# Kernel optimization log

Hardware: AMD Instinct MI355X
Metric: run time of the kernel (lower is better)

The kernel has to match this reference:

```python
import jax, jax.numpy as jnp
import numpy as np

N_SRC1, N_TGT1, N_TGT2 = 200000, 50000, 10000
E1, E2 = 1000000, 300000
F_IN, F_HID, F_OUT = 256, 192, 128


def setup_inputs() -> dict:
    key = jax.random.key(0)
    ks = jax.random.split(key, 16)
    x = jax.random.normal(ks[0], (N_SRC1, F_IN), dtype=jnp.float32)
    ei1 = jnp.stack([
        jax.random.randint(ks[1], (E1,), 0, N_SRC1, dtype=jnp.int32),
        jax.random.randint(ks[2], (E1,), 0, N_TGT1, dtype=jnp.int32),
    ])
    ei2 = jnp.stack([
        jax.random.randint(ks[3], (E2,), 0, N_TGT1, dtype=jnp.int32),
        jax.random.randint(ks[4], (E2,), 0, N_TGT2, dtype=jnp.int32),
    ])
    def w(k, o, i):
        return jax.random.normal(k, (o, i), dtype=jnp.float32) * (1.0 / np.sqrt(i))
    return {
        "x": x, "ei1": ei1, "ei2": ei2,
        "Wl1": w(ks[5], F_HID, F_IN), "bl1": jnp.zeros((F_HID,), jnp.float32), "Wr1": w(ks[6], F_HID, F_IN),
        "Wl2": w(ks[7], F_HID, F_HID), "bl2": jnp.zeros((F_HID,), jnp.float32), "Wr2": w(ks[8], F_HID, F_HID),
        "W1": w(ks[9], F_HID, F_HID), "b1": jnp.zeros((F_HID,), jnp.float32),
        "W2": w(ks[10], F_OUT, F_HID), "b2": jnp.zeros((F_OUT,), jnp.float32),
    }


def _segment_mean(feat, tgt, n):
    s = jax.ops.segment_sum(feat, tgt, num_segments=n)  # [n, d]
    c = jax.ops.segment_sum(jnp.ones((tgt.shape[0], 1), feat.dtype), tgt, num_segments=n)
    return s / jnp.maximum(c, 1.0)


def _sage_conv(x, ei, n_tgt, Wl, bl, Wr):
    # PyG SAGEConv (mean aggr): lin_l(mean of src feats per tgt) + lin_r(x_target)
    agg = _segment_mean(x[ei[0]], ei[1], n_tgt)
    return agg @ Wl.T + bl + x[:n_tgt] @ Wr.T


def reference(x, ei1, ei2, Wl1, bl1, Wr1, Wl2, bl2, Wr2, W1, b1, W2, b2):
    h = jax.nn.relu(_sage_conv(x, ei1, N_TGT1, Wl1, bl1, Wr1))   # dropout is identity in eval
    h = jax.nn.relu(_sage_conv(h, ei2, N_TGT2, Wl2, bl2, Wr2))
    embedding = h @ W1.T + b1
    h = jax.nn.relu(embedding)
    logits = h @ W2.T + b2
    return jax.nn.log_softmax(logits, axis=-1), embedding
```

## Files before the change

### kernel.cpp

```cpp
#include <hip/hip_runtime.h>
#include <hip/hip_bf16.h>

#define N_SRC1 200000
#define N_TGT1 50000
#define N_TGT2 10000
#define E1_N   1000000
#define E2_N   300000
#define F_IN   256
#define F_HID  192
#define F_OUT  128

typedef __attribute__((ext_vector_type(4))) float f32x4;
typedef __attribute__((ext_vector_type(8))) short short8;

__device__ inline float bf2f(ushort u) {
    union { uint i; float f; } c; c.i = ((uint)u) << 16; return c.f;
}
__device__ inline ushort f2bf(float f) {
    union { float f; uint i; } c; c.f = f;
    uint u = c.i;
    return (ushort)((u + 0x7FFFu + ((u >> 16) & 1u)) >> 16);
}
__device__ inline uint pack2(float a, float b) {
    return (uint)f2bf(a) | ((uint)f2bf(b) << 16);
}

#define HB1 3907
#define HB2 1172

__global__ __launch_bounds__(256) void prep(
    const float4* __restrict__ x4, uint2* __restrict__ xb,
    const float* __restrict__ Wl1, const float* __restrict__ Wr1,
    const float* __restrict__ Wl2, const float* __restrict__ Wr2,
    const float* __restrict__ W1, const float* __restrict__ W2,
    ushort* __restrict__ wc1, ushort* __restrict__ wc2,
    ushort* __restrict__ w1b, ushort* __restrict__ w2b)
{
    const int b = blockIdx.x, tid = threadIdx.x;
    if (b < 2048) {
        const int n4 = N_SRC1 * F_IN / 4;
        for (int i = b * 256 + tid; i < n4; i += 2048 * 256) {
            float4 v = x4[i];
            uint2 o;
            o.x = pack2(v.x, v.y);
            o.y = pack2(v.z, v.w);
            xb[i] = o;
        }
        return;
    }
    const int wt = (b - 2048) * 256 + tid;
    for (int idx = wt; idx < 233472; idx += 128 * 256) {
        if (idx < 98304) {
            int n = idx >> 9, k = idx & 511;
            float v = (k < 256) ? Wl1[n * 256 + k] : Wr1[n * 256 + (k - 256)];
            wc1[idx] = f2bf(v);
        } else if (idx < 98304 + 73728) {
            int i2 = idx - 98304;
            int n = i2 / 384, k = i2 - n * 384;
            float v = (k < 192) ? Wl2[n * 192 + k] : Wr2[n * 192 + (k - 192)];
            wc2[i2] = f2bf(v);
        } else if (idx < 98304 + 73728 + 36864) {
            int i3 = idx - (98304 + 73728);
            w1b[i3] = f2bf(W1[i3]);
        } else {
            int i4 = idx - (98304 + 73728 + 36864);
            w2b[i4] = f2bf(W2[i4]);
        }
    }
}

__global__ __launch_bounds__(256) void hist_kernel(
    const int* __restrict__ tgt, int* __restrict__ cnt, int E)
{
    int i = blockIdx.x * blockDim.x + threadIdx.x;
    if (i < E) atomicAdd(cnt + tgt[i], 1);
}

__global__ __launch_bounds__(256) void scan_blocks(
    const int* __restrict__ cnt, int n, int* __restrict__ off,
    int* __restrict__ partials)
{
    __shared__ int s[256];
    int tid = threadIdx.x;
    int i = blockIdx.x * 256 + tid;
    int v = (i < n) ? cnt[i] : 0;
    s[tid] = v;
    __syncthreads();
#pragma unroll
    for (int o = 1; o < 256; o <<= 1) {
        int t = (tid >= o) ? s[tid - o] : 0;
        __syncthreads();
        s[tid] += t;
        __syncthreads();
    }
    if (i < n) off[i] = s[tid] - v;
    if (tid == 255) partials[blockIdx.x] = s[255];
}

__global__ __launch_bounds__(256) void scan_partials_block(
    int* __restrict__ partials, int np, int* __restrict__ total_out)
{
    __shared__ int s[256];
    int tid = threadIdx.x;
    int v = (tid < np) ? partials[tid] : 0;
    s[tid] = v;
    __syncthreads();
#pragma unroll
    for (int o = 1; o < 256; o <<= 1) {
        int t = (tid >= o) ? s[tid - o] : 0;
        __syncthreads();
        s[tid] += t;
        __syncthreads();
    }
    if (tid < np) partials[tid] = s[tid] - v;
    if (tid == 255) *total_out = s[255];
}

__global__ __launch_bounds__(256) void add_off(
    int* __restrict__ off, const int* __restrict__ partials,
    int* __restrict__ cur, int n)
{
    int i = blockIdx.x * blockDim.x + threadIdx.x;
    if (i < n) {
        int v = off[i] + partials[i >> 8];
        off[i] = v;
        cur[i] = v;
    }
}

__global__ __launch_bounds__(256) void fill_edges(
    const int* __restrict__ src, const int* __restrict__ tgt,
    int* __restrict__ cur, int* __restrict__ esrc, int E)
{
    int i = blockIdx.x * blockDim.x + threadIdx.x;
    if (i < E) {
        int pos = atomicAdd(cur + tgt[i], 1);
        esrc[pos] = src[i];
    }
}

__global__ __launch_bounds__(256) void aggregate_bf16_256(
    const int* __restrict__ esrc, const int* __restrict__ off,
    const ushort* __restrict__ X, ushort* __restrict__ seg, int n)
{
    int wid  = blockIdx.x * 4 + (threadIdx.x >> 6);
    int lane = threadIdx.x & 63;
    if (wid >= n) return;
    int s0 = off[wid], s1 = off[wid + 1];
    float a0 = 0, a1 = 0, a2 = 0, a3 = 0;
    const uint2* base = (const uint2*)X;
    int e = s0;
    for (; e + 4 <= s1; e += 4) {
        int i0 = esrc[e], i1 = esrc[e + 1], i2 = esrc[e + 2], i3 = esrc[e + 3];
        uint2 v0 = base[(size_t)i0 * 64 + lane];
        uint2 v1 = base[(size_t)i1 * 64 + lane];
        uint2 v2 = base[(size_t)i2 * 64 + lane];
        uint2 v3 = base[(size_t)i3 * 64 + lane];
        a0 += bf2f((ushort)(v0.x & 0xffff)) + bf2f((ushort)(v1.x & 0xffff))
            + bf2f((ushort)(v2.x & 0xffff)) + bf2f((ushort)(v3.x & 0xffff));
        a1 += bf2f((ushort)(v0.x >> 16)) + bf2f((ushort)(v1.x >> 16))
            + bf2f((ushort)(v2.x >> 16)) + bf2f((ushort)(v3.x >> 16));
        a2 += bf2f((ushort)(v0.y & 0xffff)) + bf2f((ushort)(v1.y & 0xffff))
            + bf2f((ushort)(v2.y & 0xffff)) + bf2f((ushort)(v3.y & 0xffff));
        a3 += bf2f((ushort)(v0.y >> 16)) + bf2f((ushort)(v1.y >> 16))
            + bf2f((ushort)(v2.y >> 16)) + bf2f((ushort)(v3.y >> 16));
    }
    for (; e < s1; ++e) {
        uint2 v = base[(size_t)esrc[e] * 64 + lane];
        a0 += bf2f((ushort)(v.x & 0xffff)); a1 += bf2f((ushort)(v.x >> 16));
        a2 += bf2f((ushort)(v.y & 0xffff)); a3 += bf2f((ushort)(v.y >> 16));
    }
    float inv = (s1 > s0) ? 1.0f / (float)(s1 - s0) : 0.0f;
    uint2 o;
    o.x = pack2(a0 * inv, a1 * inv);
    o.y = pack2(a2 * inv, a3 * inv);
    ((uint2*)seg)[(size_t)wid * 64 + lane] = o;
}

__global__ __launch_bounds__(256) void aggregate_bf16_192(
    const int* __restrict__ esrc, const int* __restrict__ off,
    const ushort* __restrict__ X, ushort* __restrict__ seg, int n)
{
    int wid  = blockIdx.x * 4 + (threadIdx.x >> 6);
    int lane = threadIdx.x & 63;
    if (wid >= n) return;
    int s0 = off[wid], s1 = off[wid + 1];
    float a0 = 0, a1 = 0, a2 = 0, a3 = 0;
    const uint* base = (const uint*)X;
    int e = s0;
    for (; e + 4 <= s1; e += 4) {
        const uint* r0 = base + (size_t)esrc[e] * 96;
        const uint* r1 = base + (size_t)esrc[e + 1] * 96;
        const uint* r2 = base + (size_t)esrc[e + 2] * 96;
        const uint* r3 = base + (size_t)esrc[e + 3] * 96;
        uint w0 = r0[lane], w1 = r1[lane], w2 = r2[lane], w3 = r3[lane];
        a0 += bf2f((ushort)(w0 & 0xffff)) + bf2f((ushort)(w1 & 0xffff))
            + bf2f((ushort)(w2 & 0xffff)) + bf2f((ushort)(w3 & 0xffff));
        a1 += bf2f((ushort)(w0 >> 16)) + bf2f((ushort)(w1 >> 16))
            + bf2f((ushort)(w2 >> 16)) + bf2f((ushort)(w3 >> 16));
        if (lane < 32) {
            uint u0 = r0[64 + lane], u1 = r1[64 + lane],
                 u2 = r2[64 + lane], u3 = r3[64 + lane];
            a2 += bf2f((ushort)(u0 & 0xffff)) + bf2f((ushort)(u1 & 0xffff))
                + bf2f((ushort)(u2 & 0xffff)) + bf2f((ushort)(u3 & 0xffff));
            a3 += bf2f((ushort)(u0 >> 16)) + bf2f((ushort)(u1 >> 16))
                + bf2f((ushort)(u2 >> 16)) + bf2f((ushort)(u3 >> 16));
        }
    }
    for (; e < s1; ++e) {
        const uint* r = base + (size_t)esrc[e] * 96;
        uint v0 = r[lane];
        a0 += bf2f((ushort)(v0 & 0xffff)); a1 += bf2f((ushort)(v0 >> 16));
        if (lane < 32) {
            uint v1 = r[64 + lane];
            a2 += bf2f((ushort)(v1 & 0xffff)); a3 += bf2f((ushort)(v1 >> 16));
        }
    }
    float inv = (s1 > s0) ? 1.0f / (float)(s1 - s0) : 0.0f;
    uint* o = (uint*)seg + (size_t)wid * 96;
    o[lane] = pack2(a0 * inv, a1 * inv);
    if (lane < 32) o[64 + lane] = pack2(a2 * inv, a3 * inv);
}

template <int BM, int BN, int WM, int WN>
__global__ __launch_bounds__(WM * WN * 64) void gemm_mfma(
    const ushort* __restrict__ A1, int K1,
    const ushort* __restrict__ A2, int K2,
    const ushort* __restrict__ W, const float* __restrict__ bias,
    ushort* __restrict__ Cb, float* __restrict__ Cf,
    int M, int relu)
{
    constexpr int TPB = WM * WN * 64;
    constexpr int WTM = BM / WM, WTN = BN / WN;
    constexpr int MF = WTM / 16, NF = WTN / 16;
    constexpr int ROW = 40;
    __shared__ __attribute__((aligned(16))) ushort As[BM * ROW];
    __shared__ __attribute__((aligned(16))) ushort Ws[BN * ROW];
    const int tid  = threadIdx.x;
    const int lane = tid & 63;
    const int wid  = tid >> 6;
    const int wm = wid / WN, wn = wid % WN;
    const int bm = blockIdx.x * BM;
    const int K = K1 + K2;

    f32x4 acc[MF][NF];
#pragma unroll
    for (int i = 0; i < MF; ++i)
#pragma unroll
        for (int j = 0; j < NF; ++j) acc[i][j] = {0.f, 0.f, 0.f, 0.f};

    for (int k0 = 0; k0 < K; k0 += 32) {
#pragma unroll
        for (int c = tid; c < BM * 4; c += TPB) {
            int row = c >> 2, k8 = (c & 3) * 8;
            int m = bm + row, k = k0 + k8;
            uint4 v = make_uint4(0, 0, 0, 0);
            if (m < M) {
                const ushort* s = (k < K1) ? (A1 + (size_t)m * K1 + k)
                                           : (A2 + (size_t)m * K2 + (k - K1));
                v = *(const uint4*)s;
            }
            *(uint4*)&As[row * ROW + k8] = v;
        }
#pragma unroll
        for (int c = tid; c < BN * 4; c += TPB) {
            int row = c >> 2, k8 = (c & 3) * 8;
            uint4 v = *(const uint4*)(W + (size_t)row * K + k0 + k8);
            *(uint4*)&Ws[row * ROW + k8] = v;
        }
        __syncthreads();
        short8 a[MF], b[NF];
#pragma unroll
        for (int mf = 0; mf < MF; ++mf)
            a[mf] = *(const short8*)&As[(wm * WTM + mf * 16 + (lane & 15)) * ROW + (lane >> 4) * 8];
#pragma unroll
        for (int nf = 0; nf < NF; ++nf)
            b[nf] = *(const short8*)&Ws[(wn * WTN + nf * 16 + (lane & 15)) * ROW + (lane >> 4) * 8];
#pragma unroll
        for (int mf = 0; mf < MF; ++mf)
#pragma unroll
            for (int nf = 0; nf < NF; ++nf)
                acc[mf][nf] = __builtin_amdgcn_mfma_f32_16x16x32_bf16(
                    a[mf], b[nf], acc[mf][nf], 0, 0, 0);
        __syncthreads();
    }

#pragma unroll
    for (int mf = 0; mf < MF; ++mf) {
        int r0 = bm + wm * WTM + mf * 16 + (lane >> 4) * 4;
#pragma unroll
        for (int nf = 0; nf < NF; ++nf) {
            int cc = wn * WTN + nf * 16 + (lane & 15);
            float bi = bias[cc];
#pragma unroll
            for (int r = 0; r < 4; ++r) {
                int m = r0 + r;
                if (m >= M) continue;
                float v = acc[mf][nf][r] + bi;
                if (Cf) Cf[(size_t)m * BN + cc] = v;
                if (Cb) Cb[(size_t)m * BN + cc] = f2bf(relu ? fmaxf(v, 0.f) : v);
            }
        }
    }
}

__global__ __launch_bounds__(512) void tail_fused(
    const ushort* __restrict__ seg2, const ushort* __restrict__ h1,
    const ushort* __restrict__ wc2, const float* __restrict__ bl2,
    const ushort* __restrict__ w1b, const float* __restrict__ b1,
    const ushort* __restrict__ w2b, const float* __restrict__ b2,
    float* __restrict__ out_emb, float* __restrict__ out_ls, int M)
{
    __shared__ __attribute__((aligned(16))) char lds[122880];
    ushort* As0   = (ushort*)lds;
    ushort* Ws0   = (ushort*)(lds + 5120);
    ushort* h2buf = (ushort*)(lds + 20480);
    ushort* h3buf = (ushort*)(lds + 46080);
    ushort* w2buf = (ushort*)(lds + 71680);
    float*  lsbuf = (float*)(lds + 71680);

    const int tid = threadIdx.x, lane = tid & 63, wid = tid >> 6;
    const int wm = wid >> 1, wn = wid & 1;
    const int bm = blockIdx.x * 64;

    for (int c = tid; c < 128 * 24; c += 512) {
        int r = c / 24, k8 = (c % 24) * 8;
        uint4 v = *(const uint4*)(w2b + r * 192 + k8);
        *(uint4*)&w2buf[r * 200 + k8] = v;
    }

    {
        f32x4 acc[6];
#pragma unroll
        for (int j = 0; j < 6; ++j) acc[j] = {0.f, 0.f, 0.f, 0.f};
        for (int k0 = 0; k0 < 384; k0 += 32) {
            if (tid < 256) {
                int row = tid >> 2, k8 = (tid & 3) * 8;
                int m = bm + row, k = k0 + k8;
                uint4 v = make_uint4(0, 0, 0, 0);
                if (m < M) {
                    const ushort* s = (k < 192) ? (seg2 + (size_t)m * 192 + k)
                                                : (h1 + (size_t)m * 192 + (k - 192));
                    v = *(const uint4*)s;
                }
                *(uint4*)&As0[row * 40 + k8] = v;
            }
            for (int c = tid; c < 768; c += 512) {
                int row = c >> 2, k8 = (c & 3) * 8;
                uint4 v = *(const uint4*)(wc2 + (size_t)row * 384 + k0 + k8);
                *(uint4*)&Ws0[row * 40 + k8] = v;
            }
            __syncthreads();
            short8 a = *(const short8*)&As0[(wm * 16 + (lane & 15)) * 40 + (lane >> 4) * 8];
#pragma unroll
            for (int nf = 0; nf < 6; ++nf) {
                short8 b = *(const short8*)&Ws0[(wn * 96 + nf * 16 + (lane & 15)) * 40 + (lane >> 4) * 8];
                acc[nf] = __builtin_amdgcn_mfma_f32_16x16x32_bf16(a, b, acc[nf], 0, 0, 0);
            }
            __syncthreads();
        }
#pragma unroll
        for (int nf = 0; nf < 6; ++nf) {
            int cc = wn * 96 + nf * 16 + (lane & 15);
            float bi = bl2[cc];
#pragma unroll
            for (int r = 0; r < 4; ++r) {
                int row = wm * 16 + (lane >> 4) * 4 + r;
                h2buf[row * 200 + cc] = f2bf(fmaxf(acc[nf][r] + bi, 0.f));
            }
        }
    }
    __syncthreads();

    {
        f32x4 acc[6];
#pragma unroll
        for (int j = 0; j < 6; ++j) acc[j] = {0.f, 0.f, 0.f, 0.f};
        for (int k0 = 0; k0 < 192; k0 += 32) {
            for (int c = tid; c < 768; c += 512) {
                int row = c >> 2, k8 = (c & 3) * 8;
                uint4 v = *(const uint4*)(w1b + (size_t)row * 192 + k0 + k8);
                *(uint4*)&Ws0[row * 40 + k8] = v;
            }
            __syncthreads();
            short8 a = *(const short8*)&h2buf[(wm * 16 + (lane & 15)) * 200 + k0 + (lane >> 4) * 8];
#pragma unroll
            for (int nf = 0; nf < 6; ++nf) {
                short8 b = *(const short8*)&Ws0[(wn * 96 + nf * 16 + (lane & 15)) * 40 + (lane >> 4) * 8];
                acc[nf] = __builtin_amdgcn_mfma_f32_16x16x32_bf16(a, b, acc[nf], 0, 0, 0);
            }
            __syncthreads();
        }
#pragma unroll
        for (int nf = 0; nf < 6; ++nf) {
            int cc = wn * 96 + nf * 16 + (lane & 15);
            float bi = b1[cc];
#pragma unroll
            for (int r = 0; r < 4; ++r) {
                int row = wm * 16 + (lane >> 4) * 4 + r;
                int m = bm + row;
                float v = acc[nf][r] + bi;
                if (m < M) out_emb[(size_t)m * 192 + cc] = v;
                h3buf[row * 200 + cc] = f2bf(fmaxf(v, 0.f));
            }
        }
    }
    __syncthreads();

    {
        f32x4 acc[4];
#pragma unroll
        for (int j = 0; j < 4; ++j) acc[j] = {0.f, 0.f, 0.f, 0.f};
#pragma unroll
        for (int k0 = 0; k0 < 192; k0 += 32) {
            short8 a = *(const short8*)&h3buf[(wm * 16 + (lane & 15)) * 200 + k0 + (lane >> 4) * 8];
#pragma unroll
            for (int nf = 0; nf < 4; ++nf) {
                short8 b = *(const short8*)&w2buf[(wn * 64 + nf * 16 + (lane & 15)) * 200 + k0 + (lane >> 4) * 8];
                acc[nf] = __builtin_amdgcn_mfma_f32_16x16x32_bf16(a, b, acc[nf], 0, 0, 0);
            }
        }
        __syncthreads();
#pragma unroll
        for (int nf = 0; nf < 4; ++nf) {
            int cc = wn * 64 + nf * 16 + (lane & 15);
            float bi = b2[cc];
#pragma unroll
            for (int r = 0; r < 4; ++r) {
                int row = wm * 16 + (lane >> 4) * 4 + r;
                lsbuf[row * 128 + cc] = acc[nf][r] + bi;
            }
        }
    }
    __syncthreads();

    for (int i = 0; i < 8; ++i) {
        int row = wid * 8 + i;
        float a = lsbuf[row * 128 + lane], b = lsbuf[row * 128 + 64 + lane];
        float mx = fmaxf(a, b);
#pragma unroll
        for (int o = 32; o > 0; o >>= 1) mx = fmaxf(mx, __shfl_xor(mx, o));
        float s = expf(a - mx) + expf(b - mx);
#pragma unroll
        for (int o = 32; o > 0; o >>= 1) s += __shfl_xor(s, o);
        float ls = logf(s) + mx;
        int m = bm + row;
        if (m < M) {
            out_ls[(size_t)m * 128 + lane]      = a - ls;
            out_ls[(size_t)m * 128 + lane + 64] = b - ls;
        }
    }
}

extern "C" void kernel_launch(void* const* d_in, const int* in_sizes, int n_in,
                              void* d_out, int out_size, void* d_ws, size_t ws_size,
                              hipStream_t stream)
{
    const float* x   = (const float*)d_in[0];
    const int*   ei1 = (const int*)d_in[1];
    const int*   ei2 = (const int*)d_in[2];
    const float* Wl1 = (const float*)d_in[3];
    const float* bl1 = (const float*)d_in[4];
    const float* Wr1 = (const float*)d_in[5];
    const float* Wl2 = (const float*)d_in[6];
    const float* bl2 = (const float*)d_in[7];
    const float* Wr2 = (const float*)d_in[8];
    const float* W1  = (const float*)d_in[9];
    const float* b1  = (const float*)d_in[10];
    const float* W2  = (const float*)d_in[11];
    const float* b2  = (const float*)d_in[12];

    char* ws = (char*)d_ws;
    ushort* xb    = (ushort*)(ws + 0);
    ushort* seg1b = (ushort*)(ws + 102400000);
    ushort* h1b   = (ushort*)(ws + 128000000);
    int*    esrc1 = (int*)   (ws + 147200000);
    int*    cnt1  = (int*)   (ws + 151200000);
    int*    off1  = (int*)   (ws + 151400000);
    int*    part  = (int*)   (ws + 151600064);
    ushort* wc1   = (ushort*)(ws + 151601152);
    ushort* wc2   = (ushort*)(ws + 151797760);
    ushort* w1b   = (ushort*)(ws + 151945216);
    ushort* w2b   = (ushort*)(ws + 152018944);
    ushort* seg2b = (ushort*)(ws + 152068096);
    int*    esrc2 = (int*)   (ws + 147200000);
    int*    cnt2  = (int*)   (ws + 148400000);
    int*    off2  = (int*)   (ws + 148440064);

    float* out_ls  = (float*)d_out;
    float* out_emb = (float*)d_out + (size_t)N_TGT2 * F_OUT;

    const int NP1 = (N_TGT1 + 255) / 256;
    const int NP2 = (N_TGT2 + 255) / 256;

    prep<<<2176, 256, 0, stream>>>(
        (const float4*)x, (uint2*)xb, Wl1, Wr1, Wl2, Wr2, W1, W2,
        wc1, wc2, w1b, w2b);

    hipMemsetAsync(cnt1, 0, 200000, stream);
    hist_kernel<<<HB1, 256, 0, stream>>>(ei1 + E1_N, cnt1, E1_N);
    scan_blocks<<<NP1, 256, 0, stream>>>(cnt1, N_TGT1, off1, part);
    scan_partials_block<<<1, 256, 0, stream>>>(part, NP1, off1 + N_TGT1);
    add_off<<<NP1, 256, 0, stream>>>(off1, part, cnt1 , N_TGT1);
    fill_edges<<<HB1, 256, 0, stream>>>(ei1, ei1 + E1_N, cnt1, esrc1, E1_N);
    aggregate_bf16_256<<<(N_TGT1 + 3) / 4, 256, 0, stream>>>(esrc1, off1, xb, seg1b, N_TGT1);

    gemm_mfma<128, 192, 4, 2><<<(N_TGT1 + 127) / 128, 512, 0, stream>>>(
        seg1b, F_IN, xb, F_IN, wc1, bl1, h1b, nullptr, N_TGT1, 1);

    hipMemsetAsync(cnt2, 0, 40000, stream);
    hist_kernel<<<HB2, 256, 0, stream>>>(ei2 + E2_N, cnt2, E2_N);
    scan_blocks<<<NP2, 256, 0, stream>>>(cnt2, N_TGT2, off2, part);
    scan_partials_block<<<1, 256, 0, stream>>>(part, NP2, off2 + N_TGT2);
    add_off<<<NP2, 256, 0, stream>>>(off2, part, cnt2 , N_TGT2);
    fill_edges<<<HB2, 256, 0, stream>>>(ei2, ei2 + E2_N, cnt2, esrc2, E2_N);
    aggregate_bf16_192<<<(N_TGT2 + 3) / 4, 256, 0, stream>>>(esrc2, off2, h1b, seg2b, N_TGT2);

    tail_fused<<<(N_TGT2 + 63) / 64, 512, 0, stream>>>(
        seg2b, h1b, wc2, bl2, w1b, b1, w2b, b2, out_emb, out_ls, N_TGT2);
}
```

Measured before the change: 384.0 us.

## Fuse layer-1 mean aggregation into the SAGE GEMM via LDS staging

Replaces the separate layer-1 aggregation kernel and GEMM with one kernel. Each 64-row block gathers and averages neighbour features into shared memory, then runs the MFMA GEMM over the concatenated [agg, x_target] inputs. This removes the global write and re-read of the 50000x256 bf16 aggregate and one launch. In exchange the kernel uses a smaller 64-row tile, so each block re-streams the weight matrix for fewer rows, and its large LDS footprint may lower occupancy during the latency-bound gather.

```diff
diff --git a/kernel.cpp b/kernel.cpp
--- a/kernel.cpp
+++ b/kernel.cpp
@@ -139,42 +139,116 @@
     }
 }
 
-__global__ __launch_bounds__(256) void aggregate_bf16_256(
+__global__ __launch_bounds__(512) void sage1_fused(
     const int* __restrict__ esrc, const int* __restrict__ off,
-    const ushort* __restrict__ X, ushort* __restrict__ seg, int n)
-{
-    int wid  = blockIdx.x * 4 + (threadIdx.x >> 6);
-    int lane = threadIdx.x & 63;
-    if (wid >= n) return;
-    int s0 = off[wid], s1 = off[wid + 1];
-    float a0 = 0, a1 = 0, a2 = 0, a3 = 0;
-    const uint2* base = (const uint2*)X;
-    int e = s0;
-    for (; e + 4 <= s1; e += 4) {
-        int i0 = esrc[e], i1 = esrc[e + 1], i2 = esrc[e + 2], i3 = esrc[e + 3];
-        uint2 v0 = base[(size_t)i0 * 64 + lane];
-        uint2 v1 = base[(size_t)i1 * 64 + lane];
-        uint2 v2 = base[(size_t)i2 * 64 + lane];
-        uint2 v3 = base[(size_t)i3 * 64 + lane];
-        a0 += bf2f((ushort)(v0.x & 0xffff)) + bf2f((ushort)(v1.x & 0xffff))
-            + bf2f((ushort)(v2.x & 0xffff)) + bf2f((ushort)(v3.x & 0xffff));
-        a1 += bf2f((ushort)(v0.x >> 16)) + bf2f((ushort)(v1.x >> 16))
-            + bf2f((ushort)(v2.x >> 16)) + bf2f((ushort)(v3.x >> 16));
-        a2 += bf2f((ushort)(v0.y & 0xffff)) + bf2f((ushort)(v1.y & 0xffff))
-            + bf2f((ushort)(v2.y & 0xffff)) + bf2f((ushort)(v3.y & 0xffff));
-        a3 += bf2f((ushort)(v0.y >> 16)) + bf2f((ushort)(v1.y >> 16))
-            + bf2f((ushort)(v2.y >> 16)) + bf2f((ushort)(v3.y >> 16));
-    }
-    for (; e < s1; ++e) {
-        uint2 v = base[(size_t)esrc[e] * 64 + lane];
-        a0 += bf2f((ushort)(v.x & 0xffff)); a1 += bf2f((ushort)(v.x >> 16));
-        a2 += bf2f((ushort)(v.y & 0xffff)); a3 += bf2f((ushort)(v.y >> 16));
-    }
-    float inv = (s1 > s0) ? 1.0f / (float)(s1 - s0) : 0.0f;
-    uint2 o;
-    o.x = pack2(a0 * inv, a1 * inv);
-    o.y = pack2(a2 * inv, a3 * inv);
-    ((uint2*)seg)[(size_t)wid * 64 + lane] = o;
+    const ushort* __restrict__ xb, const ushort* __restrict__ W,
+    const float* __restrict__ bias, ushort* __restrict__ Cb, int M)
+{
+    constexpr int SEGP = 264;
+    __shared__ __attribute__((aligned(16))) ushort segbuf[64 * SEGP];
+    __shared__ __attribute__((aligned(16))) ushort Ws[192 * 40];
+    __shared__ __attribute__((aligned(16))) ushort As2[64 * 40];
+
+    const int tid = threadIdx.x, lane = tid & 63, wid = tid >> 6;
+    const int wm = wid >> 2, wn = wid & 3;
+    const int bm = blockIdx.x * 64;
+    const uint2* base = (const uint2*)xb;
+
+    for (int rr = 0; rr < 8; ++rr) {
+        int row = wid * 8 + rr;
+        int m = bm + row;
+        float a0 = 0, a1 = 0, a2 = 0, a3 = 0;
+        if (m < M) {
+            int s0 = off[m], s1 = off[m + 1];
+            int e = s0;
+            for (; e + 4 <= s1; e += 4) {
+                int i0 = esrc[e], i1 = esrc[e + 1], i2 = esrc[e + 2], i3 = esrc[e + 3];
+                uint2 v0 = base[(size_t)i0 * 64 + lane];
+                uint2 v1 = base[(size_t)i1 * 64 + lane];
+                uint2 v2 = base[(size_t)i2 * 64 + lane];
+                uint2 v3 = base[(size_t)i3 * 64 + lane];
+                a0 += bf2f((ushort)(v0.x & 0xffff)) + bf2f((ushort)(v1.x & 0xffff))
+                    + bf2f((ushort)(v2.x & 0xffff)) + bf2f((ushort)(v3.x & 0xffff));
+                a1 += bf2f((ushort)(v0.x >> 16)) + bf2f((ushort)(v1.x >> 16))
+                    + bf2f((ushort)(v2.x >> 16)) + bf2f((ushort)(v3.x >> 16));
+                a2 += bf2f((ushort)(v0.y & 0xffff)) + bf2f((ushort)(v1.y & 0xffff))
+                    + bf2f((ushort)(v2.y & 0xffff)) + bf2f((ushort)(v3.y & 0xffff));
+                a3 += bf2f((ushort)(v0.y >> 16)) + bf2f((ushort)(v1.y >> 16))
+                    + bf2f((ushort)(v2.y >> 16)) + bf2f((ushort)(v3.y >> 16));
+            }
+            for (; e < s1; ++e) {
+                uint2 v = base[(size_t)esrc[e] * 64 + lane];
+                a0 += bf2f((ushort)(v.x & 0xffff)); a1 += bf2f((ushort)(v.x >> 16));
+                a2 += bf2f((ushort)(v.y & 0xffff)); a3 += bf2f((ushort)(v.y >> 16));
+            }
+            float inv = (s1 > s0) ? 1.0f / (float)(s1 - s0) : 0.0f;
+            a0 *= inv; a1 *= inv; a2 *= inv; a3 *= inv;
+        }
+        uint2 o;
+        o.x = pack2(a0, a1);
+        o.y = pack2(a2, a3);
+        *(uint2*)&segbuf[row * SEGP + lane * 4] = o;
+    }
+    __syncthreads();
+
+    f32x4 acc[2][3];
+#pragma unroll
+    for (int i = 0; i < 2; ++i)
+#pragma unroll
+        for (int j = 0; j < 3; ++j) acc[i][j] = {0.f, 0.f, 0.f, 0.f};
+
+    for (int k0 = 0; k0 < 512; k0 += 32) {
+        for (int c = tid; c < 768; c += 512) {
+            int row = c >> 2, k8 = (c & 3) * 8;
+            uint4 v = *(const uint4*)(W + (size_t)row * 512 + k0 + k8);
+            *(uint4*)&Ws[row * 40 + k8] = v;
+        }
+        if (k0 >= 256 && tid < 256) {
+            int row = tid >> 2, k8 = (tid & 3) * 8;
+            int m = bm + row;
+            uint4 v = make_uint4(0, 0, 0, 0);
+            if (m < M) v = *(const uint4*)(xb + (size_t)m * 256 + (k0 - 256) + k8);
+            *(uint4*)&As2[row * 40 + k8] = v;
+        }
+        __syncthreads();
+        short8 a[2], b[3];
+        if (k0 < 256) {
+#pragma unroll
+            for (int mf = 0; mf < 2; ++mf)
+                a[mf] = *(const short8*)&segbuf[(wm * 32 + mf * 16 + (lane & 15)) * SEGP + k0 + (lane >> 4) * 8];
+        } else {
+#pragma unroll
+            for (int mf = 0; mf < 2; ++mf)
+                a[mf] = *(const short8*)&As2[(wm * 32 + mf * 16 + (lane & 15)) * 40 + (lane >> 4) * 8];
+        }
+#pragma unroll
+        for (int nf = 0; nf < 3; ++nf)
+            b[nf] = *(const short8*)&Ws[(wn * 48 + nf * 16 + (lane & 15)) * 40 + (lane >> 4) * 8];
+#pragma unroll
+        for (int mf = 0; mf < 2; ++mf)
+#pragma unroll
+            for (int nf = 0; nf < 3; ++nf)
+                acc[mf][nf] = __builtin_amdgcn_mfma_f32_16x16x32_bf16(
+                    a[mf], b[nf], acc[mf][nf], 0, 0, 0);
+        __syncthreads();
+    }
+
+#pragma unroll
+    for (int mf = 0; mf < 2; ++mf) {
+        int r0 = bm + wm * 32 + mf * 16 + (lane >> 4) * 4;
+#pragma unroll
+        for (int nf = 0; nf < 3; ++nf) {
+            int cc = wn * 48 + nf * 16 + (lane & 15);
+            float bi = bias[cc];
+#pragma unroll
+            for (int r = 0; r < 4; ++r) {
+                int m = r0 + r;
+                if (m >= M) continue;
+                float v = acc[mf][nf][r] + bi;
+                Cb[(size_t)m * 192 + cc] = f2bf(fmaxf(v, 0.f));
+            }
+        }
+    }
 }
 
 __global__ __launch_bounds__(256) void aggregate_bf16_192(
@@ -222,88 +296,6 @@
     if (lane < 32) o[64 + lane] = pack2(a2 * inv, a3 * inv);
 }
 
-template <int BM, int BN, int WM, int WN>
-__global__ __launch_bounds__(WM * WN * 64) void gemm_mfma(
-    const ushort* __restrict__ A1, int K1,
-    const ushort* __restrict__ A2, int K2,
-    const ushort* __restrict__ W, const float* __restrict__ bias,
-    ushort* __restrict__ Cb, float* __restrict__ Cf,
-    int M, int relu)
-{
-    constexpr int TPB = WM * WN * 64;
-    constexpr int WTM = BM / WM, WTN = BN / WN;
-    constexpr int MF = WTM / 16, NF = WTN / 16;
-    constexpr int ROW = 40;
-    __shared__ __attribute__((aligned(16))) ushort As[BM * ROW];
-    __shared__ __attribute__((aligned(16))) ushort Ws[BN * ROW];
-    const int tid  = threadIdx.x;
-    const int lane = tid & 63;
-    const int wid  = tid >> 6;
-    const int wm = wid / WN, wn = wid % WN;
-    const int bm = blockIdx.x * BM;
-    const int K = K1 + K2;
-
-    f32x4 acc[MF][NF];
-#pragma unroll
-    for (int i = 0; i < MF; ++i)
-#pragma unroll
-        for (int j = 0; j < NF; ++j) acc[i][j] = {0.f, 0.f, 0.f, 0.f};
-
-    for (int k0 = 0; k0 < K; k0 += 32) {
-#pragma unroll
-        for (int c = tid; c < BM * 4; c += TPB) {
-            int row = c >> 2, k8 = (c & 3) * 8;
-            int m = bm + row, k = k0 + k8;
-            uint4 v = make_uint4(0, 0, 0, 0);
-            if (m < M) {
-                const ushort* s = (k < K1) ? (A1 + (size_t)m * K1 + k)
-                                           : (A2 + (size_t)m * K2 + (k - K1));
-                v = *(const uint4*)s;
-            }
-            *(uint4*)&As[row * ROW + k8] = v;
-        }
-#pragma unroll
-        for (int c = tid; c < BN * 4; c += TPB) {
-            int row = c >> 2, k8 = (c & 3) * 8;
-            uint4 v = *(const uint4*)(W + (size_t)row * K + k0 + k8);
-            *(uint4*)&Ws[row * ROW + k8] = v;
-        }
-        __syncthreads();
-        short8 a[MF], b[NF];
-#pragma unroll
-        for (int mf = 0; mf < MF; ++mf)
-            a[mf] = *(const short8*)&As[(wm * WTM + mf * 16 + (lane & 15)) * ROW + (lane >> 4) * 8];
-#pragma unroll
-        for (int nf = 0; nf < NF; ++nf)
-            b[nf] = *(const short8*)&Ws[(wn * WTN + nf * 16 + (lane & 15)) * ROW + (lane >> 4) * 8];
-#pragma unroll
-        for (int mf = 0; mf < MF; ++mf)
-#pragma unroll
-            for (int nf = 0; nf < NF; ++nf)
-                acc[mf][nf] = __builtin_amdgcn_mfma_f32_16x16x32_bf16(
-                    a[mf], b[nf], acc[mf][nf], 0, 0, 0);
-        __syncthreads();
-    }
-
-#pragma unroll
-    for (int mf = 0; mf < MF; ++mf) {
-        int r0 = bm + wm * WTM + mf * 16 + (lane >> 4) * 4;
-#pragma unroll
-        for (int nf = 0; nf < NF; ++nf) {
-            int cc = wn * WTN + nf * 16 + (lane & 15);
-            float bi = bias[cc];
-#pragma unroll
-            for (int r = 0; r < 4; ++r) {
-                int m = r0 + r;
-                if (m >= M) continue;
-                float v = acc[mf][nf][r] + bi;
-                if (Cf) Cf[(size_t)m * BN + cc] = v;
-                if (Cb) Cb[(size_t)m * BN + cc] = f2bf(relu ? fmaxf(v, 0.f) : v);
-            }
-        }
-    }
-}
-
 __global__ __launch_bounds__(512) void tail_fused(
     const ushort* __restrict__ seg2, const ushort* __restrict__ h1,
     const ushort* __restrict__ wc2, const float* __restrict__ bl2,
@@ -472,7 +464,6 @@
 
     char* ws = (char*)d_ws;
     ushort* xb    = (ushort*)(ws + 0);
-    ushort* seg1b = (ushort*)(ws + 102400000);
     ushort* h1b   = (ushort*)(ws + 128000000);
     int*    esrc1 = (int*)   (ws + 147200000);
     int*    cnt1  = (int*)   (ws + 151200000);
@@ -503,10 +494,9 @@
     scan_partials_block<<<1, 256, 0, stream>>>(part, NP1, off1 + N_TGT1);
     add_off<<<NP1, 256, 0, stream>>>(off1, part, cnt1 , N_TGT1);
     fill_edges<<<HB1, 256, 0, stream>>>(ei1, ei1 + E1_N, cnt1, esrc1, E1_N);
-    aggregate_bf16_256<<<(N_TGT1 + 3) / 4, 256, 0, stream>>>(esrc1, off1, xb, seg1b, N_TGT1);
-
-    gemm_mfma<128, 192, 4, 2><<<(N_TGT1 + 127) / 128, 512, 0, stream>>>(
-        seg1b, F_IN, xb, F_IN, wc1, bl1, h1b, nullptr, N_TGT1, 1);
+
+    sage1_fused<<<(N_TGT1 + 63) / 64, 512, 0, stream>>>(
+        esrc1, off1, xb, wc1, bl1, h1b, N_TGT1);
 
     hipMemsetAsync(cnt2, 0, 40000, stream);
     hist_kernel<<<HB2, 256, 0, stream>>>(ei2 + E2_N, cnt2, E2_N);
```

Measured after the change: 411.0 us. 1.07x slower.
